# Kernel tuning notes

Hardware: AMD Instinct MI355X
Metric: run time of the kernel (lower is better)

The kernel has to match this reference:

```python
import jax, jax.numpy as jnp
import numpy as np

N_WIRES = 4
N_REUP = 3
N_Q_LAYERS = 2
SEQ_LEN = 10
GRU_HIDDEN = 16


def setup_inputs() -> dict:
    key = jax.random.key(0)
    ks = jax.random.split(key, 24)
    N, E = 10000, 320000
    s = 0.25
    inp = {
        'x': jax.random.normal(ks[0], (N, SEQ_LEN + 3), jnp.float32),
        'edge_index': jax.random.randint(ks[1], (2, E), 0, N, dtype=jnp.int32),
        'edge_attr': jax.random.normal(ks[2], (E, 1), jnp.float32),
        'W_ih': jax.random.normal(ks[3], (3 * GRU_HIDDEN, 1), jnp.float32) * s,
        'W_hh': jax.random.normal(ks[4], (3 * GRU_HIDDEN, GRU_HIDDEN), jnp.float32) * s,
        'b_ih': jax.random.normal(ks[5], (3 * GRU_HIDDEN,), jnp.float32) * s,
        'b_hh': jax.random.normal(ks[6], (3 * GRU_HIDDEN,), jnp.float32) * s,
        'p1_W': jax.random.normal(ks[7], (N_WIRES, GRU_HIDDEN + 3), jnp.float32) * s,
        'p1_b': jax.random.normal(ks[8], (N_WIRES,), jnp.float32) * s,
        'a1_W': jax.random.normal(ks[9], (1, 2 * N_WIRES), jnp.float32) * s,
        'q1_w': jax.random.uniform(ks[10], (N_REUP, N_Q_LAYERS, 2), jnp.float32, -np.pi, np.pi),
        'g1': jnp.ones((N_WIRES,), jnp.float32),
        'be1': jnp.zeros((N_WIRES,), jnp.float32),
        'p2_W': jax.random.normal(ks[11], (N_WIRES, N_WIRES), jnp.float32) * s,
        'p2_b': jax.random.normal(ks[12], (N_WIRES,), jnp.float32) * s,
        'a2_W': jax.random.normal(ks[13], (1, 2 * N_WIRES), jnp.float32) * s,
        'q2_w': jax.random.uniform(ks[14], (N_REUP, N_Q_LAYERS, 2), jnp.float32, -np.pi, np.pi),
        'g2': jnp.ones((N_WIRES,), jnp.float32),
        'be2': jnp.zeros((N_WIRES,), jnp.float32),
        'r_W': jax.random.normal(ks[15], (1, N_WIRES), jnp.float32) * s,
        'r_b': jax.random.normal(ks[16], (1,), jnp.float32) * s,
    }
    return inp


def _ry(theta):
    c = jnp.cos(theta * 0.5)
    s = jnp.sin(theta * 0.5)
    return jnp.stack([jnp.stack([c, -s], -1), jnp.stack([s, c], -1)], -2).astype(jnp.complex64)


def _rz(theta):
    em = jnp.exp(-0.5j * theta)
    ep = jnp.exp(0.5j * theta)
    z = jnp.zeros_like(em)
    return jnp.stack([jnp.stack([em, z], -1), jnp.stack([z, ep], -1)], -2)


def _apply1q(state, gate, wire):
    # state: [E,2,2,2,2]; gate: [2,2] shared or [E,2,2] per-edge
    st = jnp.moveaxis(state, 1 + wire, -1)
    if gate.ndim == 3:
        st = jnp.einsum('eij,e...j->e...i', gate, st)
    else:
        st = jnp.einsum('ij,e...j->e...i', gate, st)
    return jnp.moveaxis(st, -1, 1 + wire)


def _cnot(state, c, t):
    st = jnp.moveaxis(state, (1 + c, 1 + t), (-2, -1))
    st = jnp.concatenate([st[..., :1, :], st[..., 1:, ::-1]], axis=-2)
    return jnp.moveaxis(st, (-2, -1), (1 + c, 1 + t))


def _qcircuit(inputs, corr, weights):
    # inputs: [E,4] angles, corr: [E], weights: [3,2,2]; batched 4-wire statevector sim
    E = inputs.shape[0]
    state = jnp.zeros((E, 16), jnp.complex64).at[:, 0].set(1.0).reshape(E, 2, 2, 2, 2)
    for r in range(N_REUP):
        for i in range(N_WIRES):
            state = _apply1q(state, _ry(inputs[:, i]), i)
        state = _apply1q(state, _ry(corr), 0)
        for d in range(N_Q_LAYERS):
            gy = _ry(weights[r, d, 0])
            gz = _rz(weights[r, d, 1])
            for i in range(N_WIRES):
                state = _apply1q(state, gy, i)
                state = _apply1q(state, gz, i)
            for i in range(d % 2, N_WIRES - 1, 2):
                state = _cnot(state, i, i + 1)
    probs = state.real ** 2 + state.imag ** 2
    z = jnp.array([1.0, -1.0], jnp.float32)
    return jnp.stack(
        [jnp.einsum('e...j,j->e', jnp.moveaxis(probs, 1 + w, -1), z) for w in range(N_WIRES)], -1)


def _layernorm(x, g, b):
    mu = x.mean(-1, keepdims=True)
    v = ((x - mu) ** 2).mean(-1, keepdims=True)
    return (x - mu) * jax.lax.rsqrt(v + 1e-5) * g + b


def _qgat(x, edge_index, edge_attr, Wp, bp, Wa, qw, g, b):
    N = x.shape[0]
    h = jax.nn.elu(x @ Wp.T + bp)  # [N,4]
    sl = jnp.arange(N, dtype=edge_index.dtype)
    src = jnp.concatenate([edge_index[0], sl])
    dst = jnp.concatenate([edge_index[1], sl])
    ea = jnp.concatenate([edge_attr[:, 0], jnp.ones((N,), x.dtype)])
    alpha = jnp.concatenate([h[src], h[dst]], -1) @ Wa[0]  # [Et]
    alpha = jax.nn.leaky_relu(alpha, 0.2) * jnp.abs(ea)
    alpha = alpha - jax.lax.stop_gradient(alpha).max()
    aexp = jnp.exp(alpha)
    dsum = jax.ops.segment_sum(aexp, dst, num_segments=N)
    alpha = aexp / (dsum[dst] + 1e-8)
    corr = jnp.tanh(ea) * jnp.pi
    msg = alpha[:, None] * _qcircuit(jnp.tanh(h[src]) * jnp.pi, corr, qw)  # [Et,4]
    aggr = jax.ops.segment_sum(msg, dst, num_segments=N)
    return _layernorm(aggr + h, g, b)


def _gru_last(price_seq, W_ih, W_hh, b_ih, b_hh):
    # price_seq: [N,T] scalar-per-step GRU; returns final hidden [N,H]
    N = price_seq.shape[0]
    h0 = jnp.zeros((N, GRU_HIDDEN), price_seq.dtype)
    w_in = W_ih[:, 0]  # [3H]

    def step(h, x_t):
        gi = x_t[:, None] * w_in + b_ih  # [N,3H]
        gh = h @ W_hh.T + b_hh
        ir, iz, inn = jnp.split(gi, 3, -1)
        hr, hz, hn = jnp.split(gh, 3, -1)
        r = jax.nn.sigmoid(ir + hr)
        z = jax.nn.sigmoid(iz + hz)
        n = jnp.tanh(inn + r * hn)
        return (1.0 - z) * n + z * h, None

    h, _ = jax.lax.scan(step, h0, price_seq.T)
    return h


def reference(x, edge_index, edge_attr, W_ih, W_hh, b_ih, b_hh,
              p1_W, p1_b, a1_W, q1_w, g1, be1,
              p2_W, p2_b, a2_W, q2_w, g2, be2, r_W, r_b):
    hT = _gru_last(x[:, :SEQ_LEN], W_ih, W_hh, b_ih, b_hh)
    h = jnp.concatenate([hT, x[:, SEQ_LEN:]], -1)  # [N,19]
    h = jax.nn.relu(_qgat(h, edge_index, edge_attr, p1_W, p1_b, a1_W, q1_w, g1, be1))
    h = _qgat(h, edge_index, edge_attr, p2_W, p2_b, a2_W, q2_w, g2, be2)
    return (h @ r_W.T + r_b)[:, 0]
```

## Files before the change

### kernel.cpp

```cpp
#include <hip/hip_runtime.h>
#include <math.h>


#define GH 16
#define SEQ 10
#define PI_F 3.14159265358979323846f

__device__ __forceinline__ float sigmoidf_(float x) { return 1.0f / (1.0f + expf(-x)); }

template <int STR>
__device__ __forceinline__ void ry_g(float (&sr)[16], float (&si)[16], float c, float s) {
#pragma unroll
    for (int i0 = 0; i0 < 16; ++i0) {
        if (i0 & STR) continue;
        int i1 = i0 | STR;
        float a0r = sr[i0], a0i = si[i0], a1r = sr[i1], a1i = si[i1];
        sr[i0] = c * a0r - s * a1r; si[i0] = c * a0i - s * a1i;
        sr[i1] = s * a0r + c * a1r; si[i1] = s * a0i + c * a1i;
    }
}
template <int STR>
__device__ __forceinline__ void rz_g(float (&sr)[16], float (&si)[16], float c, float s) {
#pragma unroll
    for (int i = 0; i < 16; ++i) {
        float r = sr[i], im = si[i];
        if (i & STR) { sr[i] = r * c - im * s; si[i] = im * c + r * s; }
        else         { sr[i] = r * c + im * s; si[i] = im * c - r * s; }
    }
}
template <int SC, int ST>
__device__ __forceinline__ void cnot_g(float (&sr)[16], float (&si)[16]) {
#pragma unroll
    for (int i = 0; i < 16; ++i) {
        if ((i & SC) && !(i & ST)) {
            int j = i | ST;
            float tr = sr[i], ti = si[i];
            sr[i] = sr[j]; si[i] = si[j]; sr[j] = tr; si[j] = ti;
        }
    }
}

__global__ __launch_bounds__(128) void k_gmat(
    const float* __restrict__ q1w, const float* __restrict__ q2w,
    float* __restrict__ Gtab)
{
    int t = threadIdx.x;
    if (t >= 96) return;
    int layer = t / 48, rem = t % 48, rep = rem / 16, col = rem % 16;
    const float* qw = layer ? q2w : q1w;
    float sr[16], si[16];
#pragma unroll
    for (int i = 0; i < 16; ++i) { sr[i] = 0.f; si[i] = 0.f; }
    sr[col] = 1.f;
#pragma unroll
    for (int d = 0; d < 2; ++d) {
        float cy, sy, cz, sz;
        sincosf(0.5f * qw[(rep * 2 + d) * 2 + 0], &sy, &cy);
        sincosf(0.5f * qw[(rep * 2 + d) * 2 + 1], &sz, &cz);
        bool lastd = (rep == 2) && (d == 1);
        ry_g<8>(sr, si, cy, sy); if (!lastd) rz_g<8>(sr, si, cz, sz);
        ry_g<4>(sr, si, cy, sy); if (!lastd) rz_g<4>(sr, si, cz, sz);
        ry_g<2>(sr, si, cy, sy); if (!lastd) rz_g<2>(sr, si, cz, sz);
        ry_g<1>(sr, si, cy, sy); if (!lastd) rz_g<1>(sr, si, cz, sz);
        if (d == 0) { cnot_g<8, 4>(sr, si); cnot_g<2, 1>(sr, si); }
        else        { cnot_g<4, 2>(sr, si); }
    }
    float* g = Gtab + layer * 1536 + rep * 512;
#pragma unroll
    for (int i = 0; i < 16; ++i) {
        g[(i * 16 + col) * 2 + 0] = sr[i];
        g[(i * 16 + col) * 2 + 1] = si[i];
    }
}

__device__ __forceinline__ void prep_node(
    int lane, float c0, float s0, float c1, float s1,
    float c2, float s2, float c3, float s3, float hsd,
    const float (&gr)[3][16 * 17], const float (&gi)[3][16 * 17],
    float* __restrict__ Tb)
{
    float pa = (lane & 8) ? 0.f
             : ((lane & 4) ? s1 : c1) * ((lane & 2) ? s2 : c2) * ((lane & 1) ? s3 : c3);
    float pb;
    { float t = __shfl_xor(pa, 8, 16); pb = (lane & 8) ? t : -t; }

    float ar = 0.f, ai = 0.f, br = 0.f, bi = 0.f;
#pragma unroll
    for (int jj = 0; jj < 16; ++jj) {
        float Gr = gr[0][lane * 17 + jj], Gi = gi[0][lane * 17 + jj];
        float xa = __shfl(pa, jj, 16), xb = __shfl(pb, jj, 16);
        ar += Gr * xa; ai += Gi * xa; br += Gr * xb; bi += Gi * xb;
    }

#define BFLY(vr, vi, STR, cc, ss) { \
    float tr_ = __shfl_xor(vr, STR, 16), ti_ = __shfl_xor(vi, STR, 16); \
    float sg_ = (lane & STR) ? (ss) : -(ss); \
    vr = (cc) * vr + sg_ * tr_; vi = (cc) * vi + sg_ * ti_; }
#define R123(vr, vi) { BFLY(vr, vi, 4, c1, s1) BFLY(vr, vi, 2, c2, s2) BFLY(vr, vi, 1, c3, s3) }
#define KAPP(orr, oii, xr, xi) { \
    float tr_ = __shfl_xor(xr, 8, 16), ti_ = __shfl_xor(xi, 8, 16); \
    orr = (lane & 8) ? tr_ : -tr_; oii = (lane & 8) ? ti_ : -ti_; }

    R123(ar, ai) R123(br, bi)

    float sr4[4], si4[4];
    sr4[0] = ar; si4[0] = ai;
    KAPP(sr4[1], si4[1], ar, ai)
    sr4[2] = br; si4[2] = bi;
    KAPP(sr4[3], si4[3], br, bi)

    float nr4[4] = {0.f, 0.f, 0.f, 0.f}, ni4[4] = {0.f, 0.f, 0.f, 0.f};
#pragma unroll
    for (int jj = 0; jj < 16; ++jj) {
        float Gr = gr[1][lane * 17 + jj], Gi = gi[1][lane * 17 + jj];
#pragma unroll
        for (int v = 0; v < 4; ++v) {
            float xr = __shfl(sr4[v], jj, 16), xi = __shfl(si4[v], jj, 16);
            nr4[v] += Gr * xr - Gi * xi;
            ni4[v] += Gr * xi + Gi * xr;
        }
    }
#pragma unroll
    for (int v = 0; v < 4; ++v) { R123(nr4[v], ni4[v]) }

    float gr4[4], gi4[4];
    float m01r = nr4[1] + nr4[2], m01i = ni4[1] + ni4[2];
    gr4[0] = nr4[0]; gi4[0] = ni4[0];
    { float kr, ki; KAPP(kr, ki, nr4[0], ni4[0]) gr4[1] = m01r + kr; gi4[1] = m01i + ki; }
    { float kr, ki; KAPP(kr, ki, m01r, m01i)     gr4[2] = nr4[3] + kr; gi4[2] = ni4[3] + ki; }
    { float kr, ki; KAPP(kr, ki, nr4[3], ni4[3]) gr4[3] = kr; gi4[3] = ki; }

    float vr4[4] = {0.f, 0.f, 0.f, 0.f}, vi4[4] = {0.f, 0.f, 0.f, 0.f};
#pragma unroll
    for (int jj = 0; jj < 16; ++jj) {
        float Gr = gr[2][lane * 17 + jj], Gi = gi[2][lane * 17 + jj];
#pragma unroll
        for (int v = 0; v < 4; ++v) {
            float xr = __shfl(gr4[v], jj, 16), xi = __shfl(gi4[v], jj, 16);
            vr4[v] += Gr * xr - Gi * xi;
            vi4[v] += Gr * xi + Gi * xr;
        }
    }

    float p[10];
    {
        int idx = 0;
#pragma unroll
        for (int k = 0; k < 4; ++k)
#pragma unroll
            for (int l = 0; l < 4; ++l) {
                if (l < k) continue;
                p[idx++] = vr4[k] * vr4[l] + vi4[k] * vi4[l];
            }
    }
#pragma unroll
    for (int pi = 0; pi < 10; ++pi) {
        float v = p[pi];
#pragma unroll
        for (int m = 8; m >= 1; m >>= 1) {
            float t = __shfl_xor(v, m, 16);
            v = (lane & m) ? (t - v) : (v + t);
        }
        p[pi] = v;
    }

    int w = (lane == 8) ? 0 : (lane == 4) ? 1 : (lane == 2) ? 2 : (lane == 1) ? 3 : -1;
    if (w >= 0) {
#pragma unroll
        for (int pi = 0; pi < 10; ++pi) {
            float mult = (pi == 0 || pi == 4 || pi == 7 || pi == 9) ? 1.f : 2.f;
            Tb[w * 10 + pi] = mult * p[pi];
        }
    }
    if (lane == 0) { Tb[40] = c0; Tb[41] = s0; Tb[42] = hsd; Tb[43] = 0.f; }
#undef BFLY
#undef R123
#undef KAPP
}

__global__ __launch_bounds__(256) void k_gru(
    const float* __restrict__ x, const float* __restrict__ W_ih,
    const float* __restrict__ W_hh, const float* __restrict__ b_ih,
    const float* __restrict__ b_hh, const float* __restrict__ p1W,
    const float* __restrict__ p1b, const float* __restrict__ a1W,
    const float* __restrict__ Gl, const int* __restrict__ ei,
    int* __restrict__ deg, float* __restrict__ nres1,
    float* __restrict__ hdd1, float* __restrict__ T,
    float* __restrict__ Sz, int N, int E)
{
    for (int i = blockIdx.x * 256 + threadIdx.x; i < N * 10; i += gridDim.x * 256)
        Sz[i] = 0.f;
    for (int e = blockIdx.x * 256 + threadIdx.x; e < E; e += gridDim.x * 256)
        atomicAdd(&deg[ei[E + e]], 1);

    __shared__ float sW[48 * 17];
    __shared__ float sp1W[4 * 19], sp1b[4];
    __shared__ float gr[3][16 * 17], gi[3][16 * 17];
    __shared__ float sT[8 * 48];
    for (int i = threadIdx.x; i < 48 * 16; i += 256)
        sW[(i >> 4) * 17 + (i & 15)] = W_hh[i];
    if (threadIdx.x < 76) sp1W[threadIdx.x] = p1W[threadIdx.x];
    if (threadIdx.x < 4) sp1b[threadIdx.x] = p1b[threadIdx.x];
    for (int idx = threadIdx.x; idx < 3 * 256; idx += 256) {
        int rep = idx >> 8, rc = idx & 255, i = rc >> 4, jj = rc & 15;
        gr[rep][i * 17 + jj] = Gl[rep * 512 + rc * 2 + 0];
        gi[rep][i * 17 + jj] = Gl[rep * 512 + rc * 2 + 1];
    }
    __syncthreads();

    const int L = threadIdx.x & 31;
    const int j = L & 15;
    const int half = L >> 4;
    const int nib = threadIdx.x >> 5;
    const int n = blockIdx.x * 8 + nib;
    const bool valid = (n < N);

    float wr8[8], wz8[8], wn8[8];
#pragma unroll
    for (int kk = 0; kk < 8; ++kk) {
        int k = half * 8 + kk;
        wr8[kk] = sW[j * 17 + k];
        wz8[kk] = sW[(16 + j) * 17 + k];
        wn8[kk] = sW[(32 + j) * 17 + k];
    }
    float wir = W_ih[j], wiz = W_ih[16 + j], win_ = W_ih[32 + j];
    float bir = b_ih[j], biz = b_ih[16 + j], bin_ = b_ih[32 + j];
    float brr = b_hh[j], brz = b_hh[16 + j], brn = b_hh[32 + j];

    float xv[13];
#pragma unroll
    for (int t = 0; t < 13; ++t) xv[t] = valid ? x[n * 13 + t] : 0.f;

    float h = 0.f;
#pragma unroll
    for (int t = 0; t < SEQ; ++t) {
        float xt = xv[t];
        float pr = 0.f, pz = 0.f, pn = 0.f;
#pragma unroll
        for (int kk = 0; kk < 8; ++kk) {
            float hk = __shfl(h, half * 8 + kk, 16);
            pr += wr8[kk] * hk; pz += wz8[kk] * hk; pn += wn8[kk] * hk;
        }
        pr += __shfl_xor(pr, 16, 32);
        pz += __shfl_xor(pz, 16, 32);
        pn += __shfl_xor(pn, 16, 32);
        float r  = sigmoidf_(xt * wir + bir + brr + pr);
        float z  = sigmoidf_(xt * wiz + biz + brz + pz);
        float nv = tanhf(xt * win_ + bin_ + r * (brn + pn));
        h = (1.f - z) * nv + z * h;
    }

    float b0 = h * sp1W[0 * 19 + j];
    float b1 = h * sp1W[1 * 19 + j];
    float b2 = h * sp1W[2 * 19 + j];
    float b3 = h * sp1W[3 * 19 + j];
#pragma unroll
    for (int m = 1; m < 16; m <<= 1) {
        b0 += __shfl_xor(b0, m, 16);
        b1 += __shfl_xor(b1, m, 16);
        b2 += __shfl_xor(b2, m, 16);
        b3 += __shfl_xor(b3, m, 16);
    }

    float hv = 0.f, cv = 1.f, sv = 0.f, ds = 0.f, dd = 0.f;
    if (j < 4) {
        float s = (j == 0) ? b0 : (j == 1) ? b1 : (j == 2) ? b2 : b3;
        s += sp1b[j] + xv[10] * sp1W[j * 19 + 16] + xv[11] * sp1W[j * 19 + 17]
           + xv[12] * sp1W[j * 19 + 18];
        hv = (s > 0.f) ? s : expm1f(s);
        sincosf(0.5f * PI_F * tanhf(hv), &sv, &cv);
        ds = hv * a1W[j];
        dd = hv * a1W[4 + j];
    }
    ds += __shfl_xor(ds, 1, 16); ds += __shfl_xor(ds, 2, 16);
    dd += __shfl_xor(dd, 1, 16); dd += __shfl_xor(dd, 2, 16);

    float c0 = __shfl(cv, 0, 16), s0 = __shfl(sv, 0, 16);
    float c1 = __shfl(cv, 1, 16), s1 = __shfl(sv, 1, 16);
    float c2 = __shfl(cv, 2, 16), s2 = __shfl(sv, 2, 16);
    float c3 = __shfl(cv, 3, 16), s3 = __shfl(sv, 3, 16);
    float hsd = __shfl(ds, 0, 16);

    if (valid) {
        if (L < 4) nres1[n * 4 + L] = hv;
        if (L == 0) hdd1[n] = dd;
    }
    if (L < 16)
        prep_node(j, c0, s0, c1, s1, c2, s2, c3, s3, hsd, gr, gi, sT + nib * 48);
    __syncthreads();
    {
        int n0 = blockIdx.x * 8;
        int cnt = (min(n0 + 8, N) - n0) * 48;
        for (int i = threadIdx.x; i < cnt; i += 256)
            T[(size_t)n0 * 48 + i] = sT[i];
    }
}

__global__ __launch_bounds__(1024) void k_scan(
    const int* __restrict__ deg, int* __restrict__ off,
    int* __restrict__ cur, int N)
{
    __shared__ int part[1024];
    const int t = threadIdx.x;
    const int chunk = (N + 1023) / 1024;
    const int lo = t * chunk;
    const int hi = min(lo + chunk, N);
    int s = 0;
    for (int i = lo; i < hi; ++i) s += deg[i] + 1;
    part[t] = s;
    __syncthreads();
    for (int d = 1; d < 1024; d <<= 1) {
        int y = (t >= d) ? part[t - d] : 0;
        __syncthreads();
        part[t] += y;
        __syncthreads();
    }
    int run = part[t] - s;
    for (int i = lo; i < hi; ++i) { off[i] = run; cur[i] = run; run += deg[i] + 1; }
}

__global__ __launch_bounds__(256) void k_fill(
    const int* __restrict__ ei, const float* __restrict__ ea,
    int* __restrict__ cur, float4* __restrict__ rec, int E, int N)
{
    int idx = blockIdx.x * 256 + threadIdx.x;
    if (idx >= E + N) return;
    int src, d; float ev;
    if (idx < E) { src = ei[idx]; d = ei[E + idx]; ev = ea[idx]; }
    else         { src = idx - E; d = src;         ev = 1.0f;    }
    int slot = atomicAdd(&cur[d], 1);
    float scv, ccv; sincosf(0.5f * PI_F * tanhf(ev), &scv, &ccv);
    float4 r;
    r.x = __int_as_float(src | (d << 16));
    r.y = fabsf(ev);
    r.z = ccv; r.w = scv;
    rec[slot] = r;
}

__device__ __forceinline__ void segreduce(
    int dst, int lane, float a0, float a1, float a2, float a3, float a4,
    float* __restrict__ S)
{
    int prevd = __shfl_up(dst, 1);
    bool head = (lane == 0) || (prevd != dst);
    unsigned long long hm = __ballot(head);
    unsigned long long below = (2ull << lane) - 1ull;
    int H = 63 - __clzll((long long)(hm & below));
    int dist = lane - H;
#pragma unroll
    for (int st = 1; st < 64; st <<= 1) {
        float t0 = __shfl_up(a0, st), t1 = __shfl_up(a1, st),
              t2 = __shfl_up(a2, st), t3 = __shfl_up(a3, st),
              t4 = __shfl_up(a4, st);
        if (dist >= st) { a0 += t0; a1 += t1; a2 += t2; a3 += t3; a4 += t4; }
    }
    int nextd = __shfl_down(dst, 1);
    bool lastl = (lane == 63) || (dst != nextd);
    if (lastl && dst >= 0) {
        float* sbase = S + (size_t)dst * 5;
        atomicAdd(sbase + 0, a0); atomicAdd(sbase + 1, a1);
        atomicAdd(sbase + 2, a2); atomicAdd(sbase + 3, a3);
        atomicAdd(sbase + 4, a4);
    }
}

__global__ __launch_bounds__(256) void k_edge(
    const float4* __restrict__ rec, const float* __restrict__ T,
    const float* __restrict__ hdd, float* __restrict__ S, int EN)
{
    const int slot = blockIdx.x * 256 + threadIdx.x;
    const int lane = threadIdx.x & 63;
    int dst = -1;
    float acc0 = 0.f, acc1 = 0.f, acc2 = 0.f, acc3 = 0.f, acc4 = 0.f;

    if (slot < EN) {
        float4 r = rec[slot];
        int ids = __float_as_int(r.x);
        int src = ids & 0xFFFF;
        dst = ids >> 16;
        float aea = r.y, ccv = r.z, scv = r.w;

        const float* Tb = T + (size_t)src * 48;
        float t[44];
#pragma unroll
        for (int q = 0; q < 11; ++q) {
            float4 v4 = *reinterpret_cast<const float4*>(Tb + q * 4);
            t[q * 4 + 0] = v4.x; t[q * 4 + 1] = v4.y;
            t[q * 4 + 2] = v4.z; t[q * 4 + 3] = v4.w;
        }
        float hdN = hdd[dst];

        float mc = t[40] * ccv - t[41] * scv;
        float ms = t[41] * ccv + t[40] * scv;
        float m2 = mc * mc, s2 = ms * ms;
        float cf0 = mc * m2, cf1 = m2 * ms, cf2 = mc * s2, cf3 = ms * s2;
        float qq[10];
        qq[0] = cf0 * cf0; qq[1] = cf0 * cf1; qq[2] = cf0 * cf2; qq[3] = cf0 * cf3;
        qq[4] = cf1 * cf1; qq[5] = cf1 * cf2; qq[6] = cf1 * cf3;
        qq[7] = cf2 * cf2; qq[8] = cf2 * cf3; qq[9] = cf3 * cf3;

        float z0 = 0.f, z1 = 0.f, z2 = 0.f, z3 = 0.f;
#pragma unroll
        for (int pi = 0; pi < 10; ++pi) {
            z0 += t[pi] * qq[pi];
            z1 += t[10 + pi] * qq[pi];
            z2 += t[20 + pi] * qq[pi];
            z3 += t[30 + pi] * qq[pi];
        }

        float s0a = t[42] + hdN;
        s0a = (s0a > 0.f) ? s0a : 0.2f * s0a;
        float aexp = expf(s0a * aea);
        acc0 = aexp * z0; acc1 = aexp * z1; acc2 = aexp * z2; acc3 = aexp * z3;
        acc4 = aexp;
    }
    segreduce(dst, lane, acc0, acc1, acc2, acc3, acc4, S);
}

__global__ __launch_bounds__(256) void k_nodeprep(
    const float* __restrict__ S, const float* __restrict__ nres,
    const float* __restrict__ g4, const float* __restrict__ be4,
    const float* __restrict__ pW, const float* __restrict__ pb,
    const float* __restrict__ WaN, const float* __restrict__ Gl,
    float* __restrict__ onres, float* __restrict__ ohdd,
    float* __restrict__ T, int N)
{
    __shared__ float gr[3][16 * 17], gi[3][16 * 17];
    __shared__ float sT[8 * 48];
    for (int idx = threadIdx.x; idx < 3 * 256; idx += 256) {
        int rep = idx >> 8, rc = idx & 255, i = rc >> 4, jj = rc & 15;
        gr[rep][i * 17 + jj] = Gl[rep * 512 + rc * 2 + 0];
        gi[rep][i * 17 + jj] = Gl[rep * 512 + rc * 2 + 1];
    }
    __syncthreads();

    const int L = threadIdx.x & 31;
    const int j = L & 15;
    const int nib = threadIdx.x >> 5;
    const int n = blockIdx.x * 8 + nib;
    const bool valid = (n < N);

    float hv[4] = {0.f, 0.f, 0.f, 0.f};
    if (valid) {
        const float* sb = S + (size_t)n * 5;
        float dn = sb[4] + 1e-8f;
        float v0 = sb[0] / dn + nres[n * 4 + 0];
        float v1 = sb[1] / dn + nres[n * 4 + 1];
        float v2 = sb[2] / dn + nres[n * 4 + 2];
        float v3 = sb[3] / dn + nres[n * 4 + 3];
        float mu = 0.25f * (v0 + v1 + v2 + v3);
        float d0 = v0 - mu, d1 = v1 - mu, d2 = v2 - mu, d3 = v3 - mu;
        float var = 0.25f * (d0 * d0 + d1 * d1 + d2 * d2 + d3 * d3);
        float rs = 1.0f / sqrtf(var + 1e-5f);
        float y0 = fmaxf(d0 * rs * g4[0] + be4[0], 0.f);
        float y1 = fmaxf(d1 * rs * g4[1] + be4[1], 0.f);
        float y2 = fmaxf(d2 * rs * g4[2] + be4[2], 0.f);
        float y3 = fmaxf(d3 * rs * g4[3] + be4[3], 0.f);
#pragma unroll
        for (int w = 0; w < 4; ++w) {
            float s = pb[w] + y0 * pW[w * 4 + 0] + y1 * pW[w * 4 + 1]
                    + y2 * pW[w * 4 + 2] + y3 * pW[w * 4 + 3];
            hv[w] = (s > 0.f) ? s : expm1f(s);
        }
    }

    float cv = 1.f, sv = 0.f;
    if (j < 4) sincosf(0.5f * PI_F * tanhf(hv[j]), &sv, &cv);
    float c0 = __shfl(cv, 0, 16), s0 = __shfl(sv, 0, 16);
    float c1 = __shfl(cv, 1, 16), s1 = __shfl(sv, 1, 16);
    float c2 = __shfl(cv, 2, 16), s2 = __shfl(sv, 2, 16);
    float c3 = __shfl(cv, 3, 16), s3 = __shfl(sv, 3, 16);

    float hsd = hv[0] * WaN[0] + hv[1] * WaN[1] + hv[2] * WaN[2] + hv[3] * WaN[3];
    if (valid) {
        if (L < 4) onres[n * 4 + L] = hv[L];
        if (L == 0)
            ohdd[n] = hv[0] * WaN[4] + hv[1] * WaN[5] + hv[2] * WaN[6] + hv[3] * WaN[7];
    }
    if (L < 16)
        prep_node(j, c0, s0, c1, s1, c2, s2, c3, s3, hsd, gr, gi, sT + nib * 48);
    __syncthreads();
    {
        int n0 = blockIdx.x * 8;
        int cnt = (min(n0 + 8, N) - n0) * 48;
        for (int i = threadIdx.x; i < cnt; i += 256)
            T[(size_t)n0 * 48 + i] = sT[i];
    }
}

__global__ __launch_bounds__(256) void k_node2(
    const float* __restrict__ S, const float* __restrict__ nres,
    const float* __restrict__ g4, const float* __restrict__ be4,
    const float* __restrict__ rW, const float* __restrict__ rb,
    float* __restrict__ out, int N)
{
    int n = blockIdx.x * 256 + threadIdx.x;
    if (n >= N) return;
    const float* sb = S + (size_t)n * 5;
    float dn = sb[4] + 1e-8f;
    float v0 = sb[0] / dn + nres[n * 4 + 0];
    float v1 = sb[1] / dn + nres[n * 4 + 1];
    float v2 = sb[2] / dn + nres[n * 4 + 2];
    float v3 = sb[3] / dn + nres[n * 4 + 3];
    float mu = 0.25f * (v0 + v1 + v2 + v3);
    float d0 = v0 - mu, d1 = v1 - mu, d2 = v2 - mu, d3 = v3 - mu;
    float var = 0.25f * (d0 * d0 + d1 * d1 + d2 * d2 + d3 * d3);
    float rs = 1.0f / sqrtf(var + 1e-5f);
    out[n] = rb[0]
           + (d0 * rs * g4[0] + be4[0]) * rW[0]
           + (d1 * rs * g4[1] + be4[1]) * rW[1]
           + (d2 * rs * g4[2] + be4[2]) * rW[2]
           + (d3 * rs * g4[3] + be4[3]) * rW[3];
}

extern "C" void kernel_launch(void* const* d_in, const int* in_sizes, int n_in,
                              void* d_out, int out_size, void* d_ws, size_t ws_size,
                              hipStream_t stream)
{
    const float* x    = (const float*)d_in[0];
    const int*   ei   = (const int*)d_in[1];
    const float* ea   = (const float*)d_in[2];
    const float* W_ih = (const float*)d_in[3];
    const float* W_hh = (const float*)d_in[4];
    const float* b_ih = (const float*)d_in[5];
    const float* b_hh = (const float*)d_in[6];
    const float* p1W  = (const float*)d_in[7];
    const float* p1b  = (const float*)d_in[8];
    const float* a1W  = (const float*)d_in[9];
    const float* q1w  = (const float*)d_in[10];
    const float* g1   = (const float*)d_in[11];
    const float* be1  = (const float*)d_in[12];
    const float* p2W  = (const float*)d_in[13];
    const float* p2b  = (const float*)d_in[14];
    const float* a2W  = (const float*)d_in[15];
    const float* q2w  = (const float*)d_in[16];
    const float* g2   = (const float*)d_in[17];
    const float* be2  = (const float*)d_in[18];
    const float* rW   = (const float*)d_in[19];
    const float* rb   = (const float*)d_in[20];
    float* out = (float*)d_out;

    int N  = in_sizes[0] / 13;
    int E  = in_sizes[1] / 2;
    int EN = E + N;

    float* ws    = (float*)d_ws;
    float* nres1 = ws;
    float* nres2 = nres1 + (size_t)N * 4;
    float* hdd1  = nres2 + (size_t)N * 4;
    float* hdd2  = hdd1 + N;
    float* S1    = hdd2 + N;
    float* S2    = S1 + (size_t)N * 5;
    float* Gtab  = S2 + (size_t)N * 5;
    float* T     = Gtab + 3072;
    int* deg  = (int*)(T + (size_t)N * 48);
    int* off  = deg + N;
    int* cur  = off + N;
    uintptr_t rp = (uintptr_t)(cur + N);
    rp = (rp + 15u) & ~(uintptr_t)15u;
    float4* rec = (float4*)rp;

    hipMemsetAsync(deg, 0, (size_t)N * sizeof(int), stream);

    const int B = 256;
    k_gmat<<<1, 128, 0, stream>>>(q1w, q2w, Gtab);
    k_gru<<<(N + 7) / 8, B, 0, stream>>>(x, W_ih, W_hh, b_ih, b_hh, p1W, p1b,
                                         a1W, Gtab, ei, deg, nres1, hdd1, T,
                                         S1, N, E);
    k_scan<<<1, 1024, 0, stream>>>(deg, off, cur, N);
    k_fill<<<(EN + B - 1) / B, B, 0, stream>>>(ei, ea, cur, rec, E, N);

    k_edge<<<(EN + B - 1) / B, B, 0, stream>>>(rec, T, hdd1, S1, EN);
    k_nodeprep<<<(N + 7) / 8, B, 0, stream>>>(
        S1, nres1, g1, be1, p2W, p2b, a2W, Gtab + 1536, nres2, hdd2, T, N);

    k_edge<<<(EN + B - 1) / B, B, 0, stream>>>(rec, T, hdd2, S2, EN);
    k_node2<<<(N + B - 1) / B, B, 0, stream>>>(S2, nres2, g2, be2, rW, rb, out, N);
}
```

Before: 244.8 us.

## Map one node per 64-lane wavefront and split prep_node branches across lane groups

Each node now gets a full 64-lane wavefront instead of 32 lanes, 16 of which sat idle during prep_node. The four state-vector branches of the circuit simulation move into separate 16-lane groups, combined with cross-group shuffles. The GRU matvec is split four ways with an extra shuffle-reduce step. This aims to cut the serial per-lane work and the idle lanes, at the cost of twice as many blocks, more shuffles, and a whole wave spent on each node.

```diff
diff --git a/kernel.cpp b/kernel.cpp
--- a/kernel.cpp
+++ b/kernel.cpp
@@ -73,109 +73,122 @@
     }
 }
 
-__device__ __forceinline__ void prep_node(
-    int lane, float c0, float s0, float c1, float s1,
+__device__ __forceinline__ void prep_node64(
+    int L, float c0, float s0, float c1, float s1,
     float c2, float s2, float c3, float s3, float hsd,
     const float (&gr)[3][16 * 17], const float (&gi)[3][16 * 17],
     float* __restrict__ Tb)
 {
-    float pa = (lane & 8) ? 0.f
-             : ((lane & 4) ? s1 : c1) * ((lane & 2) ? s2 : c2) * ((lane & 1) ? s3 : c3);
-    float pb;
-    { float t = __shfl_xor(pa, 8, 16); pb = (lane & 8) ? t : -t; }
-
-    float ar = 0.f, ai = 0.f, br = 0.f, bi = 0.f;
+    const int i = L & 15;
+    const int g = L >> 4;
+    const float sgn = (i & 8) ? 1.f : -1.f;
+
+#define BFLY16(vr, vi, STR, cc, ss) { \
+    float tr_ = __shfl_xor(vr, STR, 16), ti_ = __shfl_xor(vi, STR, 16); \
+    float sg_ = (i & STR) ? (ss) : -(ss); \
+    vr = (cc) * vr + sg_ * tr_; vi = (cc) * vi + sg_ * ti_; }
+#define R123(vr, vi) { BFLY16(vr, vi, 4, c1, s1) BFLY16(vr, vi, 2, c2, s2) BFLY16(vr, vi, 1, c3, s3) }
+
+    float pa = (i & 8) ? 0.f
+             : ((i & 4) ? s1 : c1) * ((i & 2) ? s2 : c2) * ((i & 1) ? s3 : c3);
+    float pb = sgn * __shfl_xor(pa, 8, 16);
+
+    float src = (g < 2) ? pa : pb;
+    float vr = 0.f, vi = 0.f;
+    const int jlo = (g & 1) * 8;
+#pragma unroll
+    for (int kk = 0; kk < 8; ++kk) {
+        int jj = jlo + kk;
+        float Gr = gr[0][i * 17 + jj], Gi = gi[0][i * 17 + jj];
+        float xx = __shfl(src, jj, 16);
+        vr += Gr * xx; vi += Gi * xx;
+    }
+    vr += __shfl_xor(vr, 16);
+    vi += __shfl_xor(vi, 16);
+
+    R123(vr, vi)
+
+    {
+        float kr = sgn * __shfl_xor(vr, 8, 16);
+        float ki = sgn * __shfl_xor(vi, 8, 16);
+        if (g & 1) { vr = kr; vi = ki; }
+    }
+
+    float nr = 0.f, ni = 0.f;
 #pragma unroll
     for (int jj = 0; jj < 16; ++jj) {
-        float Gr = gr[0][lane * 17 + jj], Gi = gi[0][lane * 17 + jj];
-        float xa = __shfl(pa, jj, 16), xb = __shfl(pb, jj, 16);
-        ar += Gr * xa; ai += Gi * xa; br += Gr * xb; bi += Gi * xb;
-    }
-
-#define BFLY(vr, vi, STR, cc, ss) { \
-    float tr_ = __shfl_xor(vr, STR, 16), ti_ = __shfl_xor(vi, STR, 16); \
-    float sg_ = (lane & STR) ? (ss) : -(ss); \
-    vr = (cc) * vr + sg_ * tr_; vi = (cc) * vi + sg_ * ti_; }
-#define R123(vr, vi) { BFLY(vr, vi, 4, c1, s1) BFLY(vr, vi, 2, c2, s2) BFLY(vr, vi, 1, c3, s3) }
-#define KAPP(orr, oii, xr, xi) { \
-    float tr_ = __shfl_xor(xr, 8, 16), ti_ = __shfl_xor(xi, 8, 16); \
-    orr = (lane & 8) ? tr_ : -tr_; oii = (lane & 8) ? ti_ : -ti_; }
-
-    R123(ar, ai) R123(br, bi)
-
-    float sr4[4], si4[4];
-    sr4[0] = ar; si4[0] = ai;
-    KAPP(sr4[1], si4[1], ar, ai)
-    sr4[2] = br; si4[2] = bi;
-    KAPP(sr4[3], si4[3], br, bi)
-
-    float nr4[4] = {0.f, 0.f, 0.f, 0.f}, ni4[4] = {0.f, 0.f, 0.f, 0.f};
+        float Gr = gr[1][i * 17 + jj], Gi = gi[1][i * 17 + jj];
+        float xr = __shfl(vr, jj, 16), xi = __shfl(vi, jj, 16);
+        nr += Gr * xr - Gi * xi;
+        ni += Gr * xi + Gi * xr;
+    }
+    R123(nr, ni)
+
+    float r8  = __shfl_xor(nr, 8),  i8_ = __shfl_xor(ni, 8);
+    float r16 = __shfl_xor(nr, 16), i16 = __shfl_xor(ni, 16);
+    float r24 = __shfl_xor(nr, 24), i24 = __shfl_xor(ni, 24);
+    float r48 = __shfl_xor(nr, 48), i48 = __shfl_xor(ni, 48);
+    float r56 = __shfl_xor(nr, 56), i56 = __shfl_xor(ni, 56);
+    float br, bi;
+    if (g == 0)      { br = nr;                       bi = ni; }
+    else if (g == 1) { br = nr + r48 + sgn * r24;     bi = ni + i48 + sgn * i24; }
+    else if (g == 2) { br = r16 + sgn * (r56 + r8);   bi = i16 + sgn * (i56 + i8_); }
+    else             { br = sgn * r8;                 bi = sgn * i8_; }
+
+    float wr = 0.f, wi = 0.f;
 #pragma unroll
     for (int jj = 0; jj < 16; ++jj) {
-        float Gr = gr[1][lane * 17 + jj], Gi = gi[1][lane * 17 + jj];
-#pragma unroll
-        for (int v = 0; v < 4; ++v) {
-            float xr = __shfl(sr4[v], jj, 16), xi = __shfl(si4[v], jj, 16);
-            nr4[v] += Gr * xr - Gi * xi;
-            ni4[v] += Gr * xi + Gi * xr;
-        }
-    }
-#pragma unroll
-    for (int v = 0; v < 4; ++v) { R123(nr4[v], ni4[v]) }
-
-    float gr4[4], gi4[4];
-    float m01r = nr4[1] + nr4[2], m01i = ni4[1] + ni4[2];
-    gr4[0] = nr4[0]; gi4[0] = ni4[0];
-    { float kr, ki; KAPP(kr, ki, nr4[0], ni4[0]) gr4[1] = m01r + kr; gi4[1] = m01i + ki; }
-    { float kr, ki; KAPP(kr, ki, m01r, m01i)     gr4[2] = nr4[3] + kr; gi4[2] = ni4[3] + ki; }
-    { float kr, ki; KAPP(kr, ki, nr4[3], ni4[3]) gr4[3] = kr; gi4[3] = ki; }
-
-    float vr4[4] = {0.f, 0.f, 0.f, 0.f}, vi4[4] = {0.f, 0.f, 0.f, 0.f};
-#pragma unroll
-    for (int jj = 0; jj < 16; ++jj) {
-        float Gr = gr[2][lane * 17 + jj], Gi = gi[2][lane * 17 + jj];
-#pragma unroll
-        for (int v = 0; v < 4; ++v) {
-            float xr = __shfl(gr4[v], jj, 16), xi = __shfl(gi4[v], jj, 16);
-            vr4[v] += Gr * xr - Gi * xi;
-            vi4[v] += Gr * xi + Gi * xr;
-        }
-    }
-
-    float p[10];
-    {
-        int idx = 0;
-#pragma unroll
-        for (int k = 0; k < 4; ++k)
-#pragma unroll
-            for (int l = 0; l < 4; ++l) {
-                if (l < k) continue;
-                p[idx++] = vr4[k] * vr4[l] + vi4[k] * vi4[l];
-            }
-    }
-#pragma unroll
-    for (int pi = 0; pi < 10; ++pi) {
-        float v = p[pi];
-#pragma unroll
-        for (int m = 8; m >= 1; m >>= 1) {
-            float t = __shfl_xor(v, m, 16);
-            v = (lane & m) ? (t - v) : (v + t);
-        }
-        p[pi] = v;
-    }
-
-    int w = (lane == 8) ? 0 : (lane == 4) ? 1 : (lane == 2) ? 2 : (lane == 1) ? 3 : -1;
+        float Gr = gr[2][i * 17 + jj], Gi = gi[2][i * 17 + jj];
+        float xr = __shfl(br, jj, 16), xi = __shfl(bi, jj, 16);
+        wr += Gr * xr - Gi * xi;
+        wi += Gr * xi + Gi * xr;
+    }
+
+    float x16r = __shfl_xor(wr, 16), x16i = __shfl_xor(wi, 16);
+    float x32r = __shfl_xor(wr, 32), x32i = __shfl_xor(wi, 32);
+    float x48r = __shfl_xor(wr, 48), x48i = __shfl_xor(wi, 48);
+
+    float pA, pB, pC = 0.f;
+    int piA, piB, piC = -1;
+    bool hasC = false;
+    if (g == 0) {
+        pA = wr * wr + wi * wi;          piA = 0;
+        pB = wr * x16r + wi * x16i;      piB = 1;
+        pC = wr * x32r + wi * x32i;      piC = 2; hasC = true;
+    } else if (g == 1) {
+        pA = x16r * x32r + x16i * x32i;  piA = 3;
+        pB = wr * wr + wi * wi;          piB = 4;
+        pC = wr * x48r + wi * x48i;      piC = 5; hasC = true;
+    } else if (g == 2) {
+        pA = x48r * x16r + x48i * x16i;  piA = 6;
+        pB = wr * wr + wi * wi;          piB = 7;
+    } else {
+        pA = x16r * wr + x16i * wi;      piA = 8;
+        pB = wr * wr + wi * wi;          piB = 9;
+    }
+
+#pragma unroll
+    for (int m = 8; m >= 1; m >>= 1) {
+        float tA = __shfl_xor(pA, m, 16);
+        float tB = __shfl_xor(pB, m, 16);
+        float tC = __shfl_xor(pC, m, 16);
+        bool hi = (i & m) != 0;
+        pA = hi ? (tA - pA) : (pA + tA);
+        pB = hi ? (tB - pB) : (pB + tB);
+        pC = hi ? (tC - pC) : (pC + tC);
+    }
+
+    int w = (i == 8) ? 0 : (i == 4) ? 1 : (i == 2) ? 2 : (i == 1) ? 3 : -1;
     if (w >= 0) {
-#pragma unroll
-        for (int pi = 0; pi < 10; ++pi) {
-            float mult = (pi == 0 || pi == 4 || pi == 7 || pi == 9) ? 1.f : 2.f;
-            Tb[w * 10 + pi] = mult * p[pi];
-        }
-    }
-    if (lane == 0) { Tb[40] = c0; Tb[41] = s0; Tb[42] = hsd; Tb[43] = 0.f; }
-#undef BFLY
+        float mA = (piA == 0 || piA == 4 || piA == 7 || piA == 9) ? 1.f : 2.f;
+        float mB = (piB == 0 || piB == 4 || piB == 7 || piB == 9) ? 1.f : 2.f;
+        Tb[w * 10 + piA] = mA * pA;
+        Tb[w * 10 + piB] = mB * pB;
+        if (hasC) Tb[w * 10 + piC] = 2.f * pC;
+    }
+    if (L == 0) { Tb[40] = c0; Tb[41] = s0; Tb[42] = hsd; Tb[43] = 0.f; }
+#undef BFLY16
 #undef R123
-#undef KAPP
 }
 
 __global__ __launch_bounds__(256) void k_gru(
@@ -196,7 +209,7 @@
     __shared__ float sW[48 * 17];
     __shared__ float sp1W[4 * 19], sp1b[4];
     __shared__ float gr[3][16 * 17], gi[3][16 * 17];
-    __shared__ float sT[8 * 48];
+    __shared__ float sT[4 * 48];
     for (int i = threadIdx.x; i < 48 * 16; i += 256)
         sW[(i >> 4) * 17 + (i & 15)] = W_hh[i];
     if (threadIdx.x < 76) sp1W[threadIdx.x] = p1W[threadIdx.x];
@@ -208,89 +221,88 @@
     }
     __syncthreads();
 
-    const int L = threadIdx.x & 31;
+    const int L = threadIdx.x & 63;
     const int j = L & 15;
-    const int half = L >> 4;
-    const int nib = threadIdx.x >> 5;
-    const int n = blockIdx.x * 8 + nib;
+    const int q = L >> 4;
+    const int nw = threadIdx.x >> 6;
+    const int n = blockIdx.x * 4 + nw;
     const bool valid = (n < N);
 
-    float wr8[8], wz8[8], wn8[8];
-#pragma unroll
-    for (int kk = 0; kk < 8; ++kk) {
-        int k = half * 8 + kk;
-        wr8[kk] = sW[j * 17 + k];
-        wz8[kk] = sW[(16 + j) * 17 + k];
-        wn8[kk] = sW[(32 + j) * 17 + k];
-    }
-    float wir = W_ih[j], wiz = W_ih[16 + j], win_ = W_ih[32 + j];
-    float bir = b_ih[j], biz = b_ih[16 + j], bin_ = b_ih[32 + j];
-    float brr = b_hh[j], brz = b_hh[16 + j], brn = b_hh[32 + j];
-
-    float xv[13];
-#pragma unroll
-    for (int t = 0; t < 13; ++t) xv[t] = valid ? x[n * 13 + t] : 0.f;
-
-    float h = 0.f;
-#pragma unroll
-    for (int t = 0; t < SEQ; ++t) {
-        float xt = xv[t];
-        float pr = 0.f, pz = 0.f, pn = 0.f;
-#pragma unroll
-        for (int kk = 0; kk < 8; ++kk) {
-            float hk = __shfl(h, half * 8 + kk, 16);
-            pr += wr8[kk] * hk; pz += wz8[kk] * hk; pn += wn8[kk] * hk;
-        }
-        pr += __shfl_xor(pr, 16, 32);
-        pz += __shfl_xor(pz, 16, 32);
-        pn += __shfl_xor(pn, 16, 32);
-        float r  = sigmoidf_(xt * wir + bir + brr + pr);
-        float z  = sigmoidf_(xt * wiz + biz + brz + pz);
-        float nv = tanhf(xt * win_ + bin_ + r * (brn + pn));
-        h = (1.f - z) * nv + z * h;
-    }
-
-    float b0 = h * sp1W[0 * 19 + j];
-    float b1 = h * sp1W[1 * 19 + j];
-    float b2 = h * sp1W[2 * 19 + j];
-    float b3 = h * sp1W[3 * 19 + j];
-#pragma unroll
-    for (int m = 1; m < 16; m <<= 1) {
-        b0 += __shfl_xor(b0, m, 16);
-        b1 += __shfl_xor(b1, m, 16);
-        b2 += __shfl_xor(b2, m, 16);
-        b3 += __shfl_xor(b3, m, 16);
-    }
-
-    float hv = 0.f, cv = 1.f, sv = 0.f, ds = 0.f, dd = 0.f;
-    if (j < 4) {
-        float s = (j == 0) ? b0 : (j == 1) ? b1 : (j == 2) ? b2 : b3;
-        s += sp1b[j] + xv[10] * sp1W[j * 19 + 16] + xv[11] * sp1W[j * 19 + 17]
-           + xv[12] * sp1W[j * 19 + 18];
-        hv = (s > 0.f) ? s : expm1f(s);
-        sincosf(0.5f * PI_F * tanhf(hv), &sv, &cv);
-        ds = hv * a1W[j];
-        dd = hv * a1W[4 + j];
-    }
-    ds += __shfl_xor(ds, 1, 16); ds += __shfl_xor(ds, 2, 16);
-    dd += __shfl_xor(dd, 1, 16); dd += __shfl_xor(dd, 2, 16);
-
-    float c0 = __shfl(cv, 0, 16), s0 = __shfl(sv, 0, 16);
-    float c1 = __shfl(cv, 1, 16), s1 = __shfl(sv, 1, 16);
-    float c2 = __shfl(cv, 2, 16), s2 = __shfl(sv, 2, 16);
-    float c3 = __shfl(cv, 3, 16), s3 = __shfl(sv, 3, 16);
-    float hsd = __shfl(ds, 0, 16);
-
     if (valid) {
+        float wr4[4], wz4[4], wn4[4];
+#pragma unroll
+        for (int kk = 0; kk < 4; ++kk) {
+            int k = q * 4 + kk;
+            wr4[kk] = sW[j * 17 + k];
+            wz4[kk] = sW[(16 + j) * 17 + k];
+            wn4[kk] = sW[(32 + j) * 17 + k];
+        }
+        float wir = W_ih[j], wiz = W_ih[16 + j], win_ = W_ih[32 + j];
+        float bir = b_ih[j], biz = b_ih[16 + j], bin_ = b_ih[32 + j];
+        float brr = b_hh[j], brz = b_hh[16 + j], brn = b_hh[32 + j];
+
+        float xv[13];
+#pragma unroll
+        for (int t = 0; t < 13; ++t) xv[t] = x[n * 13 + t];
+
+        float h = 0.f;
+#pragma unroll
+        for (int t = 0; t < SEQ; ++t) {
+            float xt = xv[t];
+            float pr = 0.f, pz = 0.f, pn = 0.f;
+#pragma unroll
+            for (int kk = 0; kk < 4; ++kk) {
+                float hk = __shfl(h, q * 4 + kk, 16);
+                pr += wr4[kk] * hk; pz += wz4[kk] * hk; pn += wn4[kk] * hk;
+            }
+            pr += __shfl_xor(pr, 16); pr += __shfl_xor(pr, 32);
+            pz += __shfl_xor(pz, 16); pz += __shfl_xor(pz, 32);
+            pn += __shfl_xor(pn, 16); pn += __shfl_xor(pn, 32);
+            float r  = sigmoidf_(xt * wir + bir + brr + pr);
+            float z  = sigmoidf_(xt * wiz + biz + brz + pz);
+            float nv = tanhf(xt * win_ + bin_ + r * (brn + pn));
+            h = (1.f - z) * nv + z * h;
+        }
+
+        float b0 = h * sp1W[0 * 19 + j];
+        float b1 = h * sp1W[1 * 19 + j];
+        float b2 = h * sp1W[2 * 19 + j];
+        float b3 = h * sp1W[3 * 19 + j];
+#pragma unroll
+        for (int m = 1; m < 16; m <<= 1) {
+            b0 += __shfl_xor(b0, m, 16);
+            b1 += __shfl_xor(b1, m, 16);
+            b2 += __shfl_xor(b2, m, 16);
+            b3 += __shfl_xor(b3, m, 16);
+        }
+
+        float hv = 0.f, cv = 1.f, sv = 0.f, ds = 0.f, dd = 0.f;
+        if (j < 4) {
+            float s = (j == 0) ? b0 : (j == 1) ? b1 : (j == 2) ? b2 : b3;
+            s += sp1b[j] + xv[10] * sp1W[j * 19 + 16] + xv[11] * sp1W[j * 19 + 17]
+               + xv[12] * sp1W[j * 19 + 18];
+            hv = (s > 0.f) ? s : expm1f(s);
+            sincosf(0.5f * PI_F * tanhf(hv), &sv, &cv);
+            ds = hv * a1W[j];
+            dd = hv * a1W[4 + j];
+        }
+        ds += __shfl_xor(ds, 1, 16); ds += __shfl_xor(ds, 2, 16);
+        dd += __shfl_xor(dd, 1, 16); dd += __shfl_xor(dd, 2, 16);
+
+        float c0 = __shfl(cv, 0, 16), s0 = __shfl(sv, 0, 16);
+        float c1 = __shfl(cv, 1, 16), s1 = __shfl(sv, 1, 16);
+        float c2 = __shfl(cv, 2, 16), s2 = __shfl(sv, 2, 16);
+        float c3 = __shfl(cv, 3, 16), s3 = __shfl(sv, 3, 16);
+        float hsd = __shfl(ds, 0, 16);
+
         if (L < 4) nres1[n * 4 + L] = hv;
         if (L == 0) hdd1[n] = dd;
-    }
-    if (L < 16)
-        prep_node(j, c0, s0, c1, s1, c2, s2, c3, s3, hsd, gr, gi, sT + nib * 48);
+        prep_node64(L, c0, s0, c1, s1, c2, s2, c3, s3, hsd, gr, gi, sT + nw * 48);
+    }
     __syncthreads();
     {
-        int n0 = blockIdx.x * 8;
-        int cnt = (min(n0 + 8, N) - n0) * 48;
+        int n0 = blockIdx.x * 4;
+        int cnt = (min(n0 + 4, N) - n0) * 48;
         for (int i = threadIdx.x; i < cnt; i += 256)
             T[(size_t)n0 * 48 + i] = sT[i];
     }
@@ -426,7 +438,7 @@
     float* __restrict__ T, int N)
 {
     __shared__ float gr[3][16 * 17], gi[3][16 * 17];
-    __shared__ float sT[8 * 48];
+    __shared__ float sT[4 * 48];
     for (int idx = threadIdx.x; idx < 3 * 256; idx += 256) {
         int rep = idx >> 8, rc = idx & 255, i = rc >> 4, jj = rc & 15;
         gr[rep][i * 17 + jj] = Gl[rep * 512 + rc * 2 + 0];
@@ -434,13 +446,12 @@
     }
     __syncthreads();
 
-    const int L = threadIdx.x & 31;
+    const int L = threadIdx.x & 63;
     const int j = L & 15;
-    const int nib = threadIdx.x >> 5;
-    const int n = blockIdx.x * 8 + nib;
+    const int nw = threadIdx.x >> 6;
+    const int n = blockIdx.x * 4 + nw;
     const bool valid = (n < N);
 
-    float hv[4] = {0.f, 0.f, 0.f, 0.f};
     if (valid) {
         const float* sb = S + (size_t)n * 5;
         float dn = sb[4] + 1e-8f;
@@ -456,33 +467,44 @@
         float y1 = fmaxf(d1 * rs * g4[1] + be4[1], 0.f);
         float y2 = fmaxf(d2 * rs * g4[2] + be4[2], 0.f);
         float y3 = fmaxf(d3 * rs * g4[3] + be4[3], 0.f);
-#pragma unroll
-        for (int w = 0; w < 4; ++w) {
-            float s = pb[w] + y0 * pW[w * 4 + 0] + y1 * pW[w * 4 + 1]
-                    + y2 * pW[w * 4 + 2] + y3 * pW[w * 4 + 3];
-            hv[w] = (s > 0.f) ? s : expm1f(s);
-        }
-    }
-
-    float cv = 1.f, sv = 0.f;
-    if (j < 4) sincosf(0.5f * PI_F * tanhf(hv[j]), &sv, &cv);
-    float c0 = __shfl(cv, 0, 16), s0 = __shfl(sv, 0, 16);
-    float c1 = __shfl(cv, 1, 16), s1 = __shfl(sv, 1, 16);
-    float c2 = __shfl(cv, 2, 16), s2 = __shfl(sv, 2, 16);
-    float c3 = __shfl(cv, 3, 16), s3 = __shfl(sv, 3, 16);
-
-    float hsd = hv[0] * WaN[0] + hv[1] * WaN[1] + hv[2] * WaN[2] + hv[3] * WaN[3];
-    if (valid) {
-        if (L < 4) onres[n * 4 + L] = hv[L];
+
+        float hv0, hv1, hv2, hv3;
+        {
+            float s;
+            s = pb[0] + y0 * pW[0] + y1 * pW[1] + y2 * pW[2] + y3 * pW[3];
+            hv0 = (s > 0.f) ? s : expm1f(s);
+            s = pb[1] + y0 * pW[4] + y1 * pW[5] + y2 * pW[6] + y3 * pW[7];
+            hv1 = (s > 0.f) ? s : expm1f(s);
+            s = pb[2] + y0 * pW[8] + y1 * pW[9] + y2 * pW[10] + y3 * pW[11];
+            hv2 = (s > 0.f) ? s : expm1f(s);
+            s = pb[3] + y0 * pW[12] + y1 * pW[13] + y2 * pW[14] + y3 * pW[15];
+            hv3 = (s > 0.f) ? s : expm1f(s);
+        }
+
+        float cv = 1.f, sv = 0.f;
+        if (j < 4) {
+            float hsel = (j == 0) ? hv0 : (j == 1) ? hv1 : (j == 2) ? hv2 : hv3;
+            sincosf(0.5f * PI_F * tanhf(hsel), &sv, &cv);
+        }
+        float c0 = __shfl(cv, 0, 16), s0 = __shfl(sv, 0, 16);
+        float c1 = __shfl(cv, 1, 16), s1 = __shfl(sv, 1, 16);
+        float c2 = __shfl(cv, 2, 16), s2 = __shfl(sv, 2, 16);
+        float c3 = __shfl(cv, 3, 16), s3 = __shfl(sv, 3, 16);
+
+        float hsd = hv0 * WaN[0] + hv1 * WaN[1] + hv2 * WaN[2] + hv3 * WaN[3];
+        if (L < 4) {
+            float hsel = (L == 0) ? hv0 : (L == 1) ? hv1 : (L == 2) ? hv2 : hv3;
+            onres[n * 4 + L] = hsel;
+        }
         if (L == 0)
-            ohdd[n] = hv[0] * WaN[4] + hv[1] * WaN[5] + hv[2] * WaN[6] + hv[3] * WaN[7];
-    }
-    if (L < 16)
-        prep_node(j, c0, s0, c1, s1, c2, s2, c3, s3, hsd, gr, gi, sT + nib * 48);
+            ohdd[n] = hv0 * WaN[4] + hv1 * WaN[5] + hv2 * WaN[6] + hv3 * WaN[7];
+
+        prep_node64(L, c0, s0, c1, s1, c2, s2, c3, s3, hsd, gr, gi, sT + nw * 48);
+    }
     __syncthreads();
     {
-        int n0 = blockIdx.x * 8;
-        int cnt = (min(n0 + 8, N) - n0) * 48;
+        int n0 = blockIdx.x * 4;
+        int cnt = (min(n0 + 4, N) - n0) * 48;
         for (int i = threadIdx.x; i < cnt; i += 256)
             T[(size_t)n0 * 48 + i] = sT[i];
     }
@@ -564,14 +586,14 @@
 
     const int B = 256;
     k_gmat<<<1, 128, 0, stream>>>(q1w, q2w, Gtab);
-    k_gru<<<(N + 7) / 8, B, 0, stream>>>(x, W_ih, W_hh, b_ih, b_hh, p1W, p1b,
+    k_gru<<<(N + 3) / 4, B, 0, stream>>>(x, W_ih, W_hh, b_ih, b_hh, p1W, p1b,
                                          a1W, Gtab, ei, deg, nres1, hdd1, T,
                                          S1, N, E);
     k_scan<<<1, 1024, 0, stream>>>(deg, off, cur, N);
     k_fill<<<(EN + B - 1) / B, B, 0, stream>>>(ei, ea, cur, rec, E, N);
 
     k_edge<<<(EN + B - 1) / B, B, 0, stream>>>(rec, T, hdd1, S1, EN);
-    k_nodeprep<<<(N + 7) / 8, B, 0, stream>>>(
+    k_nodeprep<<<(N + 3) / 4, B, 0, stream>>>(
         S1, nres1, g1, be1, p2W, p2b, a2W, Gtab + 1536, nres2, hdd2, T, N);
 
     k_edge<<<(EN + B - 1) / B, B, 0, stream>>>(rec, T, hdd2, S2, EN);
```

After: 242.5 us. Within noise of the previous version (-0.9%).
